# Performance work log

Measured on AMD Instinct MI355X. Metric: run time of the kernel, lower is better.

The kernel has to match this reference:

```python
import jax, jax.numpy as jnp
import numpy as np

N_HEAD = 16
N_EMBD = 1024
HEAD_DIM = N_EMBD // N_HEAD


def setup_inputs() -> dict:
    key = jax.random.key(0)
    k1, k2, k3 = jax.random.split(key, 3)
    B, T, C = 4, 2048, N_EMBD
    scale = 1.0 / np.sqrt(C)
    x = jax.random.normal(k1, (B, T, C), dtype=jnp.float32)
    W_attn = jax.random.normal(k2, (C, 3 * C), dtype=jnp.float32) * scale
    W_proj = jax.random.normal(k3, (C, C), dtype=jnp.float32) * scale
    return {"x": x, "W_attn": W_attn, "W_proj": W_proj}


def reference(x, W_attn, W_proj):
    B, T, C = x.shape
    H, D = N_HEAD, HEAD_DIM
    qkv = x @ W_attn  # [B,T,3C]
    q, k, v = jnp.split(qkv, 3, axis=-1)
    # [B,H,T,D]
    q = q.reshape(B, T, H, D).transpose(0, 2, 1, 3)
    k = k.reshape(B, T, H, D).transpose(0, 2, 1, 3)
    v = v.reshape(B, T, H, D).transpose(0, 2, 1, 3)
    att = jnp.einsum("bhqd,bhkd->bhqk", q, k) * (1.0 / np.sqrt(D))
    mask = jnp.tril(jnp.ones((T, T), dtype=bool))
    att = jnp.where(mask, att, -jnp.inf)
    att = jax.nn.softmax(att, axis=-1)
    y = jnp.einsum("bhqk,bhkd->bhqd", att, v)
    y = y.transpose(0, 2, 1, 3).reshape(B, T, C)
    return y @ W_proj
```

## Files before the change

### kernel.cpp

```cpp
#include <hip/hip_runtime.h>
#include <hip/hip_bf16.h>

typedef __bf16 bf16x8 __attribute__((ext_vector_type(8)));
typedef __bf16 bf16x4 __attribute__((ext_vector_type(4)));
typedef float  f32x4  __attribute__((ext_vector_type(4)));

#define MFMA16(A, B, C) __builtin_amdgcn_mfma_f32_16x16x32_bf16((A), (B), (C), 0, 0, 0)

static constexpr int TB = 4;
static constexpr int TT = 2048;
static constexpr int TC = 1024;
static constexpr int TH = 16;
static constexpr int TD = 64;
static constexpr int TM = TB * TT;

__device__ __forceinline__ void gload16(const __bf16* g, __bf16* l) {
  __builtin_amdgcn_global_load_lds(
      (const __attribute__((address_space(1))) unsigned int*)g,
      (__attribute__((address_space(3))) unsigned int*)l, 16, 0, 0);
}

__global__ __launch_bounds__(256) void k_convert(const float* __restrict__ in,
                                                 __bf16* __restrict__ out, int n4) {
  int stride = gridDim.x * blockDim.x;
  for (int i = blockIdx.x * blockDim.x + threadIdx.x; i < n4; i += stride) {
    float4 v = *(const float4*)(in + (size_t)i * 4);
    bf16x4 o;
    o[0] = (__bf16)v.x; o[1] = (__bf16)v.y; o[2] = (__bf16)v.z; o[3] = (__bf16)v.w;
    *(bf16x4*)(out + (size_t)i * 4) = o;
  }
}

__global__ __launch_bounds__(256) void k_transpose_w(const float* __restrict__ w,
                                                     __bf16* __restrict__ wt,
                                                     int K, int N) {
  __shared__ __align__(16) __bf16 tile[64][72];
  const int k0 = blockIdx.y * 64, n0 = blockIdx.x * 64;
  const int tid = threadIdx.x;
#pragma unroll
  for (int it = 0; it < 4; ++it) {
    int c = tid + it * 256;
    int row = c >> 4, cc = (c & 15) * 4;
    float4 v = *(const float4*)(w + (size_t)(k0 + row) * N + n0 + cc);
    tile[row][cc + 0] = (__bf16)v.x;
    tile[row][cc + 1] = (__bf16)v.y;
    tile[row][cc + 2] = (__bf16)v.z;
    tile[row][cc + 3] = (__bf16)v.w;
  }
  __syncthreads();
#pragma unroll
  for (int it = 0; it < 2; ++it) {
    int c = tid + it * 256;
    int n = c >> 3, kk = (c & 7) * 8;
    bf16x8 v;
#pragma unroll
    for (int j = 0; j < 8; ++j) v[j] = tile[kk + j][n];
    *(bf16x8*)(wt + (size_t)(n0 + n) * K + k0 + kk) = v;
  }
}

template <int EPI>
__global__ __launch_bounds__(256, 3) void k_gemm(const __bf16* __restrict__ A,
                                                 const __bf16* __restrict__ Bt,
                                                 int N, float* __restrict__ outf,
                                                 __bf16* __restrict__ Qo,
                                                 __bf16* __restrict__ Ko,
                                                 __bf16* __restrict__ Vto) {
  __shared__ __align__(16) __bf16 As[128][32];
  __shared__ __align__(16) __bf16 Bs[128][32];
  const int gx = gridDim.x;
  const int nwg = gx * gridDim.y;
  int id = blockIdx.y * gx + blockIdx.x;
  id = (id & 7) * (nwg >> 3) + (id >> 3);
  const int bm = id / gx, bn = id % gx;
  const int tid = threadIdx.x, lane = tid & 63, wid = tid >> 6;
  const int wr = wid >> 1, wc = wid & 1;
  const int lr = lane & 15, lg = lane >> 4, lg8 = lg << 3;

  f32x4 acc[4][4];
  const f32x4 zero = {0.f, 0.f, 0.f, 0.f};
#pragma unroll
  for (int mi = 0; mi < 4; ++mi)
#pragma unroll
    for (int ni = 0; ni < 4; ++ni) acc[mi][ni] = zero;

  const __bf16* Ab = A + (size_t)bm * 128 * 1024;
  const __bf16* Bb = Bt + (size_t)bn * 128 * 1024;

  const int srow = wid * 32 + (lane >> 2);
  const int scol = (lane & 3) * 8;
  __bf16* ldsA = &As[0][0] + wid * 1024;
  __bf16* ldsB = &Bs[0][0] + wid * 1024;

  for (int k0 = 0; k0 < 1024; k0 += 32) {
    gload16(Ab + (size_t)srow * 1024 + k0 + scol, ldsA);
    gload16(Ab + (size_t)(srow + 16) * 1024 + k0 + scol, ldsA + 512);
    gload16(Bb + (size_t)srow * 1024 + k0 + scol, ldsB);
    gload16(Bb + (size_t)(srow + 16) * 1024 + k0 + scol, ldsB + 512);
    __syncthreads();

    bf16x8 af[4], bfr[4];
#pragma unroll
    for (int mi = 0; mi < 4; ++mi)
      af[mi] = *(const bf16x8*)&As[wr * 64 + mi * 16 + lr][lg8];
#pragma unroll
    for (int ni = 0; ni < 4; ++ni)
      bfr[ni] = *(const bf16x8*)&Bs[wc * 64 + ni * 16 + lr][lg8];
#pragma unroll
    for (int mi = 0; mi < 4; ++mi)
#pragma unroll
      for (int ni = 0; ni < 4; ++ni)
        acc[mi][ni] = MFMA16(af[mi], bfr[ni], acc[mi][ni]);
    __syncthreads();
  }

  const int rb = bm * 128 + wr * 64 + lg * 4;
  const int cb = bn * 128 + wc * 64 + lr;
  if constexpr (EPI == 0) {
#pragma unroll
    for (int mi = 0; mi < 4; ++mi)
#pragma unroll
      for (int ni = 0; ni < 4; ++ni)
#pragma unroll
        for (int j = 0; j < 4; ++j)
          outf[(size_t)(rb + mi * 16 + j) * N + cb + ni * 16] = acc[mi][ni][j];
  } else {
    const int which = (bn * 128) >> 10;
    if (which == 2) {
#pragma unroll
      for (int mi = 0; mi < 4; ++mi) {
        const int r0 = rb + mi * 16;
        const int b = r0 >> 11, t0 = r0 & 2047;
#pragma unroll
        for (int ni = 0; ni < 4; ++ni) {
          const int c = cb + ni * 16;
          const int h = (c & 1023) >> 6, d = c & 63;
          bf16x4 pk;
#pragma unroll
          for (int j = 0; j < 4; ++j) pk[j] = (__bf16)acc[mi][ni][j];
          *(bf16x4*)(Vto + (((size_t)(b * TH + h) * TD + d) * TT) + t0) = pk;
        }
      }
    } else {
#pragma unroll
      for (int mi = 0; mi < 4; ++mi) {
#pragma unroll
        for (int ni = 0; ni < 4; ++ni) {
#pragma unroll
          for (int j = 0; j < 4; ++j) {
            float v = acc[mi][ni][j];
            int r = rb + mi * 16 + j;
            int c = cb + ni * 16;
            int within = c & 1023;
            int h = within >> 6, d = within & 63;
            int b = r >> 11, t = r & 2047;
            size_t idx = (((size_t)(b * TH + h)) * TT + t) * TD + d;
            if (which == 0)
              Qo[idx] = (__bf16)(v * 0.125f);
            else
              Ko[idx] = (__bf16)v;
          }
        }
      }
    }
  }
}

__global__ __launch_bounds__(256, 3) void k_attn(const __bf16* __restrict__ Qg,
                                                 const __bf16* __restrict__ Kg,
                                                 const __bf16* __restrict__ Vt,
                                                 __bf16* __restrict__ Y) {
  __shared__ __align__(16) __bf16 Ksh[2][64 * 64];
  __shared__ __align__(16) __bf16 Vsh[2][64 * 64];
  __shared__ __align__(16) __bf16 Plds[4][16][64];
  const int flat = blockIdx.x + (blockIdx.y << 4);
  const int W = (flat & 7) * 128 + (flat >> 3);
  const int bh = W >> 4, p = W & 15;
  const int tid = threadIdx.x, lane = tid & 63, w = tid >> 6;
  const int lr = lane & 15, lg = lane >> 4, lg8 = lg << 3, lg4 = lg << 2;

  const __bf16* Qb = Qg + ((size_t)bh * TT) * TD;
  const __bf16* Kb = Kg + ((size_t)bh * TT) * TD;
  const __bf16* Vb = Vt + ((size_t)bh * TD) * TT;
  const int b = bh >> 4, hh = bh & 15;
  __bf16* Yb = Y + ((size_t)b * TT) * TC + hh * TD;

  const int c0 = p, c1 = 31 - p;
  const int nkt0 = c0 + 1;
  const int nt = nkt0 + c1 + 1;

  constexpr float LOG2E = 1.44269504f;
  constexpr float CM = 12.0f * LOG2E;
  const f32x4 zero = {0.f, 0.f, 0.f, 0.f};

  auto STAGE = [&](int bb, int kb) {
#pragma unroll
    for (int it = 0; it < 2; ++it) {
      int slot = tid + (it << 8);
      int r = slot >> 3;
      int sc = (slot & 7) ^ (r & 7);
      gload16(Kb + (size_t)(kb + r) * TD + sc * 8, &Ksh[bb][(it << 11) + (w << 9)]);
      gload16(Vb + (size_t)r * TT + kb + sc * 8, &Vsh[bb][(it << 11) + (w << 9)]);
    }
  };

  int off[4][2];
#pragma unroll
  for (int i = 0; i < 4; ++i)
#pragma unroll
    for (int h = 0; h < 2; ++h)
      off[i][h] = (i * 16 + lr) * 64 + ((((h << 2) + lg) ^ (lr & 7)) << 3);

  int wOff[4];
#pragma unroll
  for (int kf = 0; kf < 4; ++kf)
    wOff[kf] = ((((kf << 1) + (lg >> 1)) ^ (lr & 7)) << 3) + ((lg & 1) << 2);
  const int rOff0 = (lg ^ (lr & 7)) << 3;
  const int rOff1 = ((4 + lg) ^ (lr & 7)) << 3;

  int qw = c0 * 64 + w * 16;
  bf16x8 qf[2];
#pragma unroll
  for (int h = 0; h < 2; ++h)
    qf[h] = *(const bf16x8*)(Qb + (size_t)(qw + lr) * TD + h * 32 + lg8);
  f32x4 o[4];
  f32x4 l4 = zero;
#pragma unroll
  for (int df = 0; df < 4; ++df) o[df] = zero;

  auto epilogue = [&]() {
    float L = (l4[0] + l4[1]) + (l4[2] + l4[3]);
    L += __shfl_xor(L, 16);
    L += __shfl_xor(L, 32);
    const float inv = 1.0f / L;
#pragma unroll
    for (int j = 0; j < 4; ++j) {
      const float invr = __shfl(inv, lg4 + j);
      const int row = qw + lg4 + j;
#pragma unroll
      for (int df = 0; df < 4; ++df)
        Yb[(size_t)row * TC + df * 16 + lr] = (__bf16)(o[df][j] * invr);
    }
  };

  int cur = 0;
  STAGE(0, 0);
  __syncthreads();

  for (int t = 0; t < nt; ++t) {
    if (t + 1 < nt) {
      int t2 = t + 1;
      int kb2 = (t2 < nkt0 ? t2 : t2 - nkt0) << 6;
      STAGE(cur ^ 1, kb2);
    }
    if (t == nkt0) {
      epilogue();
      qw = c1 * 64 + w * 16;
#pragma unroll
      for (int h = 0; h < 2; ++h)
        qf[h] = *(const bf16x8*)(Qb + (size_t)(qw + lr) * TD + h * 32 + lg8);
      l4 = zero;
#pragma unroll
      for (int df = 0; df < 4; ++df) o[df] = zero;
    }

    const int kb = (t < nkt0 ? t : t - nkt0) << 6;
    const __bf16* Kt = Ksh[cur];
    const __bf16* Vst = Vsh[cur];

    bf16x8 kA[4][2];
#pragma unroll
    for (int kf = 0; kf < 4; ++kf)
#pragma unroll
      for (int h = 0; h < 2; ++h)
        kA[kf][h] = *(const bf16x8*)&Kt[off[kf][h]];

    f32x4 s4[4];
    __builtin_amdgcn_s_setprio(1);
#pragma unroll
    for (int kf = 0; kf < 4; ++kf) {
      f32x4 z = zero;
      z = MFMA16(kA[kf][0], qf[0], z);
      z = MFMA16(kA[kf][1], qf[1], z);
      s4[kf] = z;
    }
    __builtin_amdgcn_s_setprio(0);

    bf16x8 vB[4][2];
#pragma unroll
    for (int df = 0; df < 4; ++df)
#pragma unroll
      for (int h = 0; h < 2; ++h)
        vB[df][h] = *(const bf16x8*)&Vst[off[df][h]];

    {
      const int q = qw + lr;
      const bool diag = (kb + 63 > qw);
#pragma unroll
      for (int kf = 0; kf < 4; ++kf) {
#pragma unroll
        for (int j = 0; j < 4; ++j) {
          float arg = __builtin_fmaf(s4[kf][j], LOG2E, -CM);
          if (diag) {
            int key = kb + kf * 16 + lg4 + j;
            if (key > q) arg = -16384.0f;
          }
          s4[kf][j] = __builtin_amdgcn_exp2f(arg);
        }
        l4 += s4[kf];
        bf16x4 pk;
#pragma unroll
        for (int j = 0; j < 4; ++j) pk[j] = (__bf16)s4[kf][j];
        *(bf16x4*)&Plds[w][lr][wOff[kf]] = pk;
      }
    }

    __builtin_amdgcn_s_setprio(1);
    {
      bf16x8 pa0 = *(const bf16x8*)&Plds[w][lr][rOff0];
      bf16x8 pa1 = *(const bf16x8*)&Plds[w][lr][rOff1];
#pragma unroll
      for (int df = 0; df < 4; ++df) {
        o[df] = MFMA16(pa0, vB[df][0], o[df]);
        o[df] = MFMA16(pa1, vB[df][1], o[df]);
      }
    }
    __builtin_amdgcn_s_setprio(0);

    __syncthreads();
    cur ^= 1;
  }

  epilogue();
}

extern "C" void kernel_launch(void* const* d_in, const int* in_sizes, int n_in,
                              void* d_out, int out_size, void* d_ws, size_t ws_size,
                              hipStream_t stream) {
  const float* x  = (const float*)d_in[0];
  const float* Wa = (const float*)d_in[1];
  const float* Wp = (const float*)d_in[2];
  float* out = (float*)d_out;

  char* ws = (char*)d_ws;
  size_t off = 0;
  auto alloc = [&](size_t bytes) { char* p = ws + off; off += bytes; return p; };
  __bf16* xb   = (__bf16*)alloc((size_t)TM * TC * 2);
  __bf16* wat  = (__bf16*)alloc((size_t)3 * TC * TC * 2);
  __bf16* wpt  = (__bf16*)alloc((size_t)TC * TC * 2);
  __bf16* Qb   = (__bf16*)alloc((size_t)TM * TC * 2);
  __bf16* Kb   = (__bf16*)alloc((size_t)TM * TC * 2);
  __bf16* Vtb  = (__bf16*)alloc((size_t)TM * TC * 2);
  __bf16* Yb   = xb;

  k_convert<<<2048, 256, 0, stream>>>(x, xb, (TM * TC) / 4);
  k_transpose_w<<<dim3(48, 16), 256, 0, stream>>>(Wa, wat, 1024, 3072);
  k_transpose_w<<<dim3(16, 16), 256, 0, stream>>>(Wp, wpt, 1024, 1024);
  k_gemm<1><<<dim3(24, 64), 256, 0, stream>>>(xb, wat, 3072, nullptr, Qb, Kb, Vtb);
  k_attn<<<dim3(16, 64), 256, 0, stream>>>(Qb, Kb, Vtb, Yb);
  k_gemm<0><<<dim3(8, 64), 256, 0, stream>>>(Yb, wpt, 1024, out, nullptr, nullptr, nullptr);
}
```

Measured before the change: 176.3 us.

## Double GEMM K-tile to 64 with XOR-swizzled LDS layout

Raises the GEMM K-step from 32 to 64, which halves the number of barrier pairs and loop iterations across the K dimension. Applies an XOR swizzle to the column chunk in the global-to-LDS loads and to the fragment reads so that LDS bank conflicts are reduced. LDS per block doubles to 32KB, which may limit the 3-blocks-per-CU occupancy target, and register pressure rises because fragments for two K sub-steps are held at once.

```diff
diff --git a/kernel.cpp b/kernel.cpp
--- a/kernel.cpp
+++ b/kernel.cpp
@@ -66,8 +66,8 @@
                                                  __bf16* __restrict__ Qo,
                                                  __bf16* __restrict__ Ko,
                                                  __bf16* __restrict__ Vto) {
-  __shared__ __align__(16) __bf16 As[128][32];
-  __shared__ __align__(16) __bf16 Bs[128][32];
+  __shared__ __align__(16) __bf16 As[128 * 64];
+  __shared__ __align__(16) __bf16 Bs[128 * 64];
   const int gx = gridDim.x;
   const int nwg = gx * gridDim.y;
   int id = blockIdx.y * gx + blockIdx.x;
@@ -75,7 +75,7 @@
   const int bm = id / gx, bn = id % gx;
   const int tid = threadIdx.x, lane = tid & 63, wid = tid >> 6;
   const int wr = wid >> 1, wc = wid & 1;
-  const int lr = lane & 15, lg = lane >> 4, lg8 = lg << 3;
+  const int lr = lane & 15, lg = lane >> 4;
 
   f32x4 acc[4][4];
   const f32x4 zero = {0.f, 0.f, 0.f, 0.f};
@@ -87,30 +87,43 @@
   const __bf16* Ab = A + (size_t)bm * 128 * 1024;
   const __bf16* Bb = Bt + (size_t)bn * 128 * 1024;
 
-  const int srow = wid * 32 + (lane >> 2);
-  const int scol = (lane & 3) * 8;
-  __bf16* ldsA = &As[0][0] + wid * 1024;
-  __bf16* ldsB = &Bs[0][0] + wid * 1024;
-
-  for (int k0 = 0; k0 < 1024; k0 += 32) {
-    gload16(Ab + (size_t)srow * 1024 + k0 + scol, ldsA);
-    gload16(Ab + (size_t)(srow + 16) * 1024 + k0 + scol, ldsA + 512);
-    gload16(Bb + (size_t)srow * 1024 + k0 + scol, ldsB);
-    gload16(Bb + (size_t)(srow + 16) * 1024 + k0 + scol, ldsB + 512);
+  const int rr = wid * 8 + (lane >> 3);
+  const int sc = (lane & 7) ^ (lane >> 3);
+
+  int offA[4][2], offB[4][2];
+#pragma unroll
+  for (int i = 0; i < 4; ++i)
+#pragma unroll
+    for (int kk = 0; kk < 2; ++kk) {
+      const int xo = ((((kk << 2) + lg) ^ (lr & 7)) << 3);
+      offA[i][kk] = (wr * 64 + i * 16 + lr) * 64 + xo;
+      offB[i][kk] = (wc * 64 + i * 16 + lr) * 64 + xo;
+    }
+
+  for (int k0 = 0; k0 < 1024; k0 += 64) {
+#pragma unroll
+    for (int it = 0; it < 4; ++it) {
+      const int r = it * 32 + rr;
+      gload16(Ab + (size_t)r * 1024 + k0 + sc * 8, As + it * 2048 + wid * 512);
+      gload16(Bb + (size_t)r * 1024 + k0 + sc * 8, Bs + it * 2048 + wid * 512);
+    }
     __syncthreads();
 
-    bf16x8 af[4], bfr[4];
+    bf16x8 af[4][2], bfr[4][2];
 #pragma unroll
     for (int mi = 0; mi < 4; ++mi)
-      af[mi] = *(const bf16x8*)&As[wr * 64 + mi * 16 + lr][lg8];
-#pragma unroll
-    for (int ni = 0; ni < 4; ++ni)
-      bfr[ni] = *(const bf16x8*)&Bs[wc * 64 + ni * 16 + lr][lg8];
+#pragma unroll
+      for (int kk = 0; kk < 2; ++kk) {
+        af[mi][kk]  = *(const bf16x8*)&As[offA[mi][kk]];
+        bfr[mi][kk] = *(const bf16x8*)&Bs[offB[mi][kk]];
+      }
 #pragma unroll
     for (int mi = 0; mi < 4; ++mi)
 #pragma unroll
-      for (int ni = 0; ni < 4; ++ni)
-        acc[mi][ni] = MFMA16(af[mi], bfr[ni], acc[mi][ni]);
+      for (int ni = 0; ni < 4; ++ni) {
+        acc[mi][ni] = MFMA16(af[mi][0], bfr[ni][0], acc[mi][ni]);
+        acc[mi][ni] = MFMA16(af[mi][1], bfr[ni][1], acc[mi][ni]);
+      }
     __syncthreads();
   }
 
```

New measurement: 163.2 us. 7.4% less time.

## Double-buffer GEMM LDS tiles and XOR-swizzle layout to avoid bank conflicts

Applied to the files above, without the earlier changes.

The projection GEMM kernel now uses two LDS buffers per operand, so the next K-slice's global-to-LDS loads are issued before the MFMAs on the current slice, with one barrier per iteration. LDS columns are XOR-swizzled on store and matching offsets are precomputed for fragment reads, meant to reduce bank conflicts. This doubles shared memory per block, which may lower occupancy under the 3-blocks-per-CU launch bound. With only one barrier there is a possible race: the async global_load_lds writes into the alternate buffer may not be waited on before the barrier, depending on how the compiler inserts vmcnt waits.

```diff
diff --git a/kernel.cpp b/kernel.cpp
--- a/kernel.cpp
+++ b/kernel.cpp
@@ -66,8 +66,8 @@
                                                  __bf16* __restrict__ Qo,
                                                  __bf16* __restrict__ Ko,
                                                  __bf16* __restrict__ Vto) {
-  __shared__ __align__(16) __bf16 As[128][32];
-  __shared__ __align__(16) __bf16 Bs[128][32];
+  __shared__ __align__(16) __bf16 As[2][128 * 32];
+  __shared__ __align__(16) __bf16 Bs[2][128 * 32];
   const int gx = gridDim.x;
   const int nwg = gx * gridDim.y;
   int id = blockIdx.y * gx + blockIdx.x;
@@ -75,7 +75,7 @@
   const int bm = id / gx, bn = id % gx;
   const int tid = threadIdx.x, lane = tid & 63, wid = tid >> 6;
   const int wr = wid >> 1, wc = wid & 1;
-  const int lr = lane & 15, lg = lane >> 4, lg8 = lg << 3;
+  const int lr = lane & 15, lg = lane >> 4;
 
   f32x4 acc[4][4];
   const f32x4 zero = {0.f, 0.f, 0.f, 0.f};
@@ -87,31 +87,46 @@
   const __bf16* Ab = A + (size_t)bm * 128 * 1024;
   const __bf16* Bb = Bt + (size_t)bn * 128 * 1024;
 
-  const int srow = wid * 32 + (lane >> 2);
-  const int scol = (lane & 3) * 8;
-  __bf16* ldsA = &As[0][0] + wid * 1024;
-  __bf16* ldsB = &Bs[0][0] + wid * 1024;
+  const int srow0 = wid * 16 + (lane >> 2);
+  const int ssc = (lane & 3) ^ ((lane >> 2) & 3);
+  auto STAGE = [&](int bb, int k0) {
+#pragma unroll
+    for (int it = 0; it < 2; ++it) {
+      const int r = it * 64 + srow0;
+      gload16(Ab + (size_t)r * 1024 + k0 + ssc * 8, &As[bb][it * 2048 + wid * 512]);
+      gload16(Bb + (size_t)r * 1024 + k0 + ssc * 8, &Bs[bb][it * 2048 + wid * 512]);
+    }
+  };
+
+  int offA[4], offB[4];
+#pragma unroll
+  for (int i = 0; i < 4; ++i) {
+    const int xo = ((lg ^ (lr & 3)) << 3);
+    offA[i] = (wr * 64 + i * 16 + lr) * 32 + xo;
+    offB[i] = (wc * 64 + i * 16 + lr) * 32 + xo;
+  }
+
+  int cur = 0;
+  STAGE(0, 0);
+  __syncthreads();
 
   for (int k0 = 0; k0 < 1024; k0 += 32) {
-    gload16(Ab + (size_t)srow * 1024 + k0 + scol, ldsA);
-    gload16(Ab + (size_t)(srow + 16) * 1024 + k0 + scol, ldsA + 512);
-    gload16(Bb + (size_t)srow * 1024 + k0 + scol, ldsB);
-    gload16(Bb + (size_t)(srow + 16) * 1024 + k0 + scol, ldsB + 512);
-    __syncthreads();
+    if (k0 + 32 < 1024) STAGE(cur ^ 1, k0 + 32);
 
     bf16x8 af[4], bfr[4];
 #pragma unroll
-    for (int mi = 0; mi < 4; ++mi)
-      af[mi] = *(const bf16x8*)&As[wr * 64 + mi * 16 + lr][lg8];
-#pragma unroll
-    for (int ni = 0; ni < 4; ++ni)
-      bfr[ni] = *(const bf16x8*)&Bs[wc * 64 + ni * 16 + lr][lg8];
+    for (int mi = 0; mi < 4; ++mi) {
+      af[mi]  = *(const bf16x8*)&As[cur][offA[mi]];
+      bfr[mi] = *(const bf16x8*)&Bs[cur][offB[mi]];
+    }
 #pragma unroll
     for (int mi = 0; mi < 4; ++mi)
 #pragma unroll
       for (int ni = 0; ni < 4; ++ni)
         acc[mi][ni] = MFMA16(af[mi], bfr[ni], acc[mi][ni]);
+
     __syncthreads();
+    cur ^= 1;
   }
 
   const int rb = bm * 128 + wr * 64 + lg * 4;
```

Result: no change. 175.2 us (-0.6%).
